# Optimization experiments

Hardware: AMD Instinct MI355X
Metric: run time of the kernel (lower is better)

The kernel has to match this reference:

```python
import jax, jax.numpy as jnp
import numpy as np

TAU = 2.0
HEADS = 8

@jax.custom_vjp
def heaviside(x):
    return (x >= 0).astype(x.dtype)

def _hv_fwd(x):
    return (x >= 0).astype(x.dtype), x

def _hv_bwd(x, g):
    # spikingjelly default surrogate: sigmoid, alpha=4
    s = jax.nn.sigmoid(4.0 * x)
    return (g * 4.0 * s * (1.0 - s),)

heaviside.defvjp(_hv_fwd, _hv_bwd)

def lif(x, v_th=1.0):
    # MultiStepLIFNode(tau=2, v_reset=0, detach_reset, hard reset); x: [T, ...]
    def step(v, xt):
        v = v + (xt - v) / TAU
        s = heaviside(v - v_th)
        v = v * (1.0 - jax.lax.stop_gradient(s))
        return v, s
    _, spikes = jax.lax.scan(step, jnp.zeros_like(x[0]), x)
    return spikes

def bn_c(x, p, eps=1e-5):
    # eval-mode BatchNorm over channel axis 2; p rows: gamma, beta, mean, var
    sh = [1] * x.ndim
    sh[2] = p.shape[1]
    g, b, m, v = (p[i].reshape(sh) for i in range(4))
    return g * (x - m) * jax.lax.rsqrt(v + eps) + b

def setup_inputs():
    key = jax.random.key(0)
    ks = jax.random.split(key, 17)
    T, B, C, H, W = 4, 16, 256, 32, 32
    Hd = 4 * C
    f = lambda k, sh, sc: jax.random.normal(k, sh, jnp.float32) * sc
    u = lambda k, sh: jax.random.uniform(k, sh, jnp.float32)
    return {
        "x": f(ks[0], (T, B, C, H, W), 1.0),
        "res_attn": jnp.zeros((1,), jnp.float32),
        "wq": f(ks[1], (C, C), C ** -0.5),
        "bn_q": u(ks[2], (4, C)),
        "wk": f(ks[3], (C, C), C ** -0.5),
        "bn_k": u(ks[4], (4, C)),
        "wv": f(ks[5], (C, C), C ** -0.5),
        "bn_v": u(ks[6], (4, C)),
        "w_proj": f(ks[7], (C, C), C ** -0.5),
        "b_proj": f(ks[8], (C,), 0.02),
        "bn_proj": u(ks[9], (4, C)),
        "w_fc1": f(ks[10], (Hd, C), C ** -0.5),
        "b_fc1": f(ks[11], (Hd,), 0.02),
        "bn_fc1": u(ks[12], (4, Hd)),
        "w_fc2": f(ks[13], (C, Hd), Hd ** -0.5),
        "b_fc2": f(ks[14], (C,), 0.02),
        "bn_fc2": u(ks[15], (4, C)),
    }

def reference(x, res_attn, wq, bn_q, wk, bn_k, wv, bn_v, w_proj, b_proj, bn_proj,
              w_fc1, b_fc1, bn_fc1, w_fc2, b_fc2, bn_fc2):
    T, B, C, H, W = x.shape
    N = H * W
    d = C // HEADS
    scale = 0.125
    xf = x.reshape(T, B, C, N)

    def qkv(w, bnp):
        y = jnp.einsum('oc,tbcn->tbon', w, xf)  # conv1x1, no bias
        return lif(bn_c(y, bnp))

    # [T,B,C,N] -> [T,B,h,N,d]; channel c = h*d + di (matches torch reshape)
    to_heads = lambda t: t.reshape(T, B, HEADS, d, N).transpose(0, 1, 2, 4, 3)
    q = to_heads(qkv(wq, bn_q))
    k = to_heads(qkv(wk, bn_k))
    v = to_heads(qkv(wv, bn_v))

    kv = jnp.einsum('tbhnd,tbhne->tbhde', k, v)          # [T,B,h,d,d]
    a = jnp.einsum('tbhnd,tbhde->tbhne', q, kv) * scale  # [T,B,h,N,d]
    a = a.transpose(0, 1, 2, 4, 3).reshape(T, B, C, N)   # transpose(3,4)+reshape
    a = lif(a, v_th=0.5)                                 # attn_lif

    p = jnp.einsum('oc,tbcn->tbon', w_proj, a) + b_proj[None, None, :, None]
    attn_out = lif(bn_c(p, bn_proj).reshape(T, B, C, H, W))

    x = x + attn_out

    h1 = jnp.einsum('oc,tbchw->tbohw', w_fc1, x) + b_fc1[None, None, :, None, None]
    h1 = lif(bn_c(h1, bn_fc1))
    h2 = jnp.einsum('co,tbohw->tbchw', w_fc2, h1) + b_fc2[None, None, :, None, None]
    mlp_out = lif(bn_c(h2, bn_fc2))

    return x + mlp_out
```

## Files before the change

kernel.cpp:

```cpp
#include <hip/hip_runtime.h>
#include <stdint.h>

#define T_ 4
#define B_ 16
#define C_ 256
#define N_ 1024
#define HD_ 1024
#define HEADS_ 8
#define DH_ 32

typedef float v2f __attribute__((ext_vector_type(2)));

#define PKL(a, w, x) asm("v_pk_fma_f32 %0, %1, %2, %0 op_sel:[0,0,0] op_sel_hi:[0,1,1]" : "+v"(a) : "v"(w), "v"(x))
#define PKH(a, w, x) asm("v_pk_fma_f32 %0, %1, %2, %0 op_sel:[1,0,0] op_sel_hi:[1,1,1]" : "+v"(a) : "v"(w), "v"(x))

__global__ __launch_bounds__(256)
void transW(const float* __restrict__ W, float* __restrict__ Wt,
            int O, int K, int ostride, int ooff)
{
  __shared__ float tl[32][33];
  int k0 = blockIdx.x*32, o0 = blockIdx.y*32;
  int tid = threadIdx.x;
  int a = tid & 31, bq = tid >> 5;
#pragma unroll
  for (int i=0;i<4;i++)
    tl[bq+8*i][a] = W[(size_t)(o0+bq+8*i)*K + k0 + a];
  __syncthreads();
#pragma unroll
  for (int i=0;i<4;i++)
    Wt[(size_t)(k0+bq+8*i)*ostride + ooff + o0 + a] = tl[a][bq+8*i];
}

__global__ __launch_bounds__(256)
void packBn3(const float* __restrict__ a, const float* __restrict__ b,
             const float* __restrict__ c, float* __restrict__ o)
{
  int i = blockIdx.x*256 + threadIdx.x;
  int r = i >> 8, ci = i & 255;
  o[(size_t)r*768 + ci]       = a[i];
  o[(size_t)r*768 + 256 + ci] = b[i];
  o[(size_t)r*768 + 512 + ci] = c[i];
}

template<typename T> struct VecT;
template<> struct VecT<float>  { using t = float4; };
template<> struct VecT<uint8_t>{ using t = uchar4; };
__device__ __forceinline__ float4 cvt4(float4 v){ return v; }
__device__ __forceinline__ float4 cvt4(uchar4 u){
  return make_float4((float)u.x,(float)u.y,(float)u.z,(float)u.w);
}

template<int KDIM,int ODIM,bool HAS_BIAS,int MODE,typename TIn>
__global__ __launch_bounds__(256,2)
void vec_gemm(const TIn* __restrict__ X, const float* __restrict__ Wt,
              const float* __restrict__ bias, const float* __restrict__ bn,
              const float* __restrict__ resid, void* __restrict__ out, float vth)
{
  using XV = typename VecT<TIn>::t;
  constexpr int NC = KDIM/16;
  __shared__ __align__(16) float Xs[16*128];
  __shared__ __align__(16) float Ws[16*128];

  const int tid = threadIdx.x;
  const int tx = tid & 15, ty = tid >> 4;
  const int b = blockIdx.z, o0 = blockIdx.y*128, n0 = blockIdx.x*128;
  const int sk = tid >> 4, sc = (tid & 15)*8;

  v2f vli[8][4];
#pragma unroll
  for (int i=0;i<8;i++)
#pragma unroll
    for (int j=0;j<4;j++) vli[i][j] = (v2f){0.f,0.f};

  float4 wr0 = *(const float4*)&Wt[(size_t)sk*ODIM + o0+sc];
  float4 wr1 = *(const float4*)&Wt[(size_t)sk*ODIM + o0+sc+4];
  XV xr0 = *(const XV*)(X + (size_t)b*KDIM*N_ + (size_t)sk*N_ + n0+sc);
  XV xr1 = *(const XV*)(X + (size_t)b*KDIM*N_ + (size_t)sk*N_ + n0+sc+4);

  for (int t=0;t<T_;t++){
    v2f acc[8][4];
#pragma unroll
    for (int i=0;i<8;i++)
#pragma unroll
      for (int j=0;j<4;j++) acc[i][j] = (v2f){0.f,0.f};

    for (int c=0;c<NC;c++){
      __syncthreads();
      *(float4*)&Ws[sk*128+sc]   = wr0;
      *(float4*)&Ws[sk*128+sc+4] = wr1;
      *(float4*)&Xs[sk*128+sc]   = cvt4(xr0);
      *(float4*)&Xs[sk*128+sc+4] = cvt4(xr1);
      __syncthreads();
      {
        int nt = t, nc = c+1;
        if (nc==NC){ nc=0; nt=t+1; }
        if (nt<T_){
          const TIn* Xn = X + (size_t)(nt*B_+b)*KDIM*N_;
          wr0 = *(const float4*)&Wt[(size_t)(nc*16+sk)*ODIM + o0+sc];
          wr1 = *(const float4*)&Wt[(size_t)(nc*16+sk)*ODIM + o0+sc+4];
          xr0 = *(const XV*)(Xn + (size_t)(nc*16+sk)*N_ + n0+sc);
          xr1 = *(const XV*)(Xn + (size_t)(nc*16+sk)*N_ + n0+sc+4);
        }
      }
#pragma unroll
      for (int k=0;k<16;k++){
        v2f wa = *(const v2f*)&Ws[k*128 + 8*ty];
        v2f wb = *(const v2f*)&Ws[k*128 + 8*ty + 2];
        v2f wc = *(const v2f*)&Ws[k*128 + 8*ty + 4];
        v2f wd = *(const v2f*)&Ws[k*128 + 8*ty + 6];
        v2f xf[4];
        xf[0] = *(const v2f*)&Xs[k*128 + tx*4];
        xf[1] = *(const v2f*)&Xs[k*128 + tx*4 + 2];
        xf[2] = *(const v2f*)&Xs[k*128 + 64 + tx*4];
        xf[3] = *(const v2f*)&Xs[k*128 + 64 + tx*4 + 2];
#pragma unroll
        for (int j=0;j<4;j++){
          PKL(acc[0][j], wa, xf[j]);
          PKH(acc[1][j], wa, xf[j]);
          PKL(acc[2][j], wb, xf[j]);
          PKH(acc[3][j], wb, xf[j]);
          PKL(acc[4][j], wc, xf[j]);
          PKH(acc[5][j], wc, xf[j]);
          PKL(acc[6][j], wd, xf[j]);
          PKH(acc[7][j], wd, xf[j]);
        }
      }
    }
#pragma unroll
    for (int i=0;i<8;i++){
      int o = o0 + 8*ty + i;
      float g  = bn[o];
      float be = bn[ODIM + o];
      float m  = bn[2*ODIM + o];
      float rs = 1.0f / sqrtf(bn[3*ODIM + o] + 1e-5f);
      float bi = HAS_BIAS ? bias[o] : 0.0f;
      float sv[8];
#pragma unroll
      for (int jj=0;jj<8;jj++){
        float y  = acc[i][jj>>1][jj&1] + bi;
        float yb = (g*(y - m))*rs + be;
        float vv = vli[i][jj>>1][jj&1];
        vv += (yb - vv)*0.5f;
        float s = (vv >= vth) ? 1.0f : 0.0f;
        vli[i][jj>>1][jj&1] = (s!=0.0f) ? 0.0f : vv;
        sv[jj] = s;
      }
      size_t base = ((size_t)(t*B_+b)*ODIM + o)*N_ + n0;
      if (MODE==0){
        uchar4 pa, pb;
        pa.x=(uint8_t)sv[0]; pa.y=(uint8_t)sv[1]; pa.z=(uint8_t)sv[2]; pa.w=(uint8_t)sv[3];
        pb.x=(uint8_t)sv[4]; pb.y=(uint8_t)sv[5]; pb.z=(uint8_t)sv[6]; pb.w=(uint8_t)sv[7];
        *(uchar4*)((uint8_t*)out + base + tx*4)      = pa;
        *(uchar4*)((uint8_t*)out + base + 64 + tx*4) = pb;
      } else {
        float4 r0 = *(const float4*)&resid[base + tx*4];
        float4 r1 = *(const float4*)&resid[base + 64 + tx*4];
        float4 w0 = make_float4(r0.x+sv[0], r0.y+sv[1], r0.z+sv[2], r0.w+sv[3]);
        float4 w1 = make_float4(r1.x+sv[4], r1.y+sv[5], r1.z+sv[6], r1.w+sv[7]);
        *(float4*)&((float*)out)[base + tx*4]      = w0;
        *(float4*)&((float*)out)[base + 64 + tx*4] = w1;
      }
    }
  }
}

__global__ __launch_bounds__(256)
void kv_kernel(const uint8_t* __restrict__ qkv, float* __restrict__ kvout)
{
  int blk = blockIdx.x;
  int h = blk & 7, tb = blk >> 3;
  int tid = threadIdx.x;
  int e = tid & 31, d0 = (tid >> 5) * 4;
  const uint8_t* kp = qkv + ((size_t)tb*768 + 256 + h*DH_)*N_;
  const uint8_t* vp = qkv + ((size_t)tb*768 + 512 + h*DH_)*N_;
  const uint4* vr = (const uint4*)(vp + (size_t)e*N_);
  const uint4* k0 = (const uint4*)(kp + (size_t)(d0+0)*N_);
  const uint4* k1 = (const uint4*)(kp + (size_t)(d0+1)*N_);
  const uint4* k2 = (const uint4*)(kp + (size_t)(d0+2)*N_);
  const uint4* k3 = (const uint4*)(kp + (size_t)(d0+3)*N_);
  int s0=0,s1=0,s2=0,s3=0;
  for (int q=0;q<N_/16;q++){
    uint4 vv = vr[q];
    uint4 a0 = k0[q], a1 = k1[q], a2 = k2[q], a3 = k3[q];
    s0 += __popc(a0.x&vv.x)+__popc(a0.y&vv.y)+__popc(a0.z&vv.z)+__popc(a0.w&vv.w);
    s1 += __popc(a1.x&vv.x)+__popc(a1.y&vv.y)+__popc(a1.z&vv.z)+__popc(a1.w&vv.w);
    s2 += __popc(a2.x&vv.x)+__popc(a2.y&vv.y)+__popc(a2.z&vv.z)+__popc(a2.w&vv.w);
    s3 += __popc(a3.x&vv.x)+__popc(a3.y&vv.y)+__popc(a3.z&vv.z)+__popc(a3.w&vv.w);
  }
  float* kvp = kvout + (size_t)blk*DH_*DH_;
  kvp[(d0+0)*DH_ + e] = (float)s0;
  kvp[(d0+1)*DH_ + e] = (float)s1;
  kvp[(d0+2)*DH_ + e] = (float)s2;
  kvp[(d0+3)*DH_ + e] = (float)s3;
}

__global__ __launch_bounds__(256)
void attn_lif_kernel(const uint8_t* __restrict__ qkv, const float* __restrict__ kv,
                     uint8_t* __restrict__ as_)
{
  int tid = threadIdx.x;
  int n = blockIdx.x*256 + tid;
  int h = blockIdx.y, b = blockIdx.z;
  __shared__ float kvL[DH_*DH_];
  float v[DH_];
#pragma unroll
  for (int e=0;e<DH_;e++) v[e]=0.0f;
  for (int t=0;t<T_;t++){
    const float* kvp = kv + ((size_t)((t*B_+b)*HEADS_+h))*DH_*DH_;
    __syncthreads();
#pragma unroll
    for (int r=0;r<4;r++) kvL[tid+256*r] = kvp[tid+256*r];
    __syncthreads();
    const uint8_t* qp = qkv + ((size_t)(t*B_+b)*768 + h*DH_)*N_ + n;
    float qv[DH_];
#pragma unroll
    for (int d=0;d<DH_;d++) qv[d] = (float)qp[(size_t)d*N_];
    uint8_t* op = as_ + ((size_t)(t*B_+b)*C_ + h*DH_)*N_ + n;
#pragma unroll
    for (int e=0;e<DH_;e++){
      float a=0.0f;
#pragma unroll
      for (int d=0;d<DH_;d++) a += qv[d]*kvL[d*DH_+e];
      a *= 0.125f;
      float vv = v[e];
      vv += (a - vv)*0.5f;
      float s = (vv >= 0.5f) ? 1.0f : 0.0f;
      v[e] = (s!=0.0f) ? 0.0f : vv;
      op[(size_t)e*N_] = (uint8_t)s;
    }
  }
}

extern "C" void kernel_launch(void* const* d_in, const int* in_sizes, int n_in,
                              void* d_out, int out_size, void* d_ws, size_t ws_size,
                              hipStream_t stream)
{
  const float* x      = (const float*)d_in[0];
  const float* wq     = (const float*)d_in[2];
  const float* bn_q   = (const float*)d_in[3];
  const float* wk     = (const float*)d_in[4];
  const float* bn_k   = (const float*)d_in[5];
  const float* wv     = (const float*)d_in[6];
  const float* bn_v   = (const float*)d_in[7];
  const float* wproj  = (const float*)d_in[8];
  const float* bproj  = (const float*)d_in[9];
  const float* bnproj = (const float*)d_in[10];
  const float* wfc1   = (const float*)d_in[11];
  const float* bfc1   = (const float*)d_in[12];
  const float* bnfc1  = (const float*)d_in[13];
  const float* wfc2   = (const float*)d_in[14];
  const float* bfc2   = (const float*)d_in[15];
  const float* bnfc2  = (const float*)d_in[16];

  char* ws = (char*)d_ws;
  const size_t TB = (size_t)T_*B_;
  uint8_t* qkv = (uint8_t*)ws;
  uint8_t* as_ = (uint8_t*)ws + TB*768*N_;
  uint8_t* h1s = (uint8_t*)ws;
  size_t off = TB*768*N_ + TB*(size_t)C_*N_;
  float* xnew = (float*)(ws + off); off += TB*(size_t)C_*N_*4;
  float* WtQ  = (float*)(ws + off); off += (size_t)C_*768*4;
  float* WtP  = (float*)(ws + off); off += (size_t)C_*C_*4;
  float* WtF1 = (float*)(ws + off); off += (size_t)C_*HD_*4;
  float* WtF2 = (float*)(ws + off); off += (size_t)HD_*C_*4;
  float* bnQ  = (float*)(ws + off); off += 4*768*4;
  float* kvb  = (float*)(ws + off); off += TB*HEADS_*DH_*DH_*4;

  dim3 blk(256);
  transW<<<dim3(8,8),blk,0,stream>>>(wq, WtQ, 256, 256, 768, 0);
  transW<<<dim3(8,8),blk,0,stream>>>(wk, WtQ, 256, 256, 768, 256);
  transW<<<dim3(8,8),blk,0,stream>>>(wv, WtQ, 256, 256, 768, 512);
  transW<<<dim3(8,8),blk,0,stream>>>(wproj, WtP, 256, 256, 256, 0);
  transW<<<dim3(8,32),blk,0,stream>>>(wfc1, WtF1, 1024, 256, 1024, 0);
  transW<<<dim3(32,8),blk,0,stream>>>(wfc2, WtF2, 256, 1024, 256, 0);
  packBn3<<<dim3(4),blk,0,stream>>>(bn_q, bn_k, bn_v, bnQ);

  vec_gemm<C_,768,false,0,float><<<dim3(8,6,16),blk,0,stream>>>(
      x, WtQ, nullptr, bnQ, nullptr, qkv, 1.0f);
  kv_kernel<<<dim3(T_*B_*HEADS_),blk,0,stream>>>(qkv, kvb);
  attn_lif_kernel<<<dim3(4,HEADS_,B_),blk,0,stream>>>(qkv, kvb, as_);
  vec_gemm<C_,C_,true,1,uint8_t><<<dim3(8,2,16),blk,0,stream>>>(
      as_, WtP, bproj, bnproj, x, xnew, 1.0f);
  vec_gemm<C_,HD_,true,0,float><<<dim3(8,8,16),blk,0,stream>>>(
      xnew, WtF1, bfc1, bnfc1, nullptr, h1s, 1.0f);
  vec_gemm<HD_,C_,true,1,uint8_t><<<dim3(8,2,16),blk,0,stream>>>(
      h1s, WtF2, bfc2, bnfc2, xnew, d_out, 1.0f);
}
```

Before: 1.539 ms.

## Rewrite pointwise GEMMs to use scalar-register weights and async LDS-staged activations

The register-blocked GEMM with both operands staged in LDS is replaced. In the new kernel each wavefront holds 8 or 16 output-channel weights in scalar registers, loaded with s_load, and applies them to 4 spatial columns per lane with packed FMAs. Activations are double-buffered in LDS through global_load_lds, so the separate register round-trip and LDS store of the weight tile go away. This cuts LDS traffic and VGPR pressure so occupancy can rise to 3 blocks, but each lane now does less work per loaded value and relies on hand-written waitcnt and inline asm being correct.

```diff
diff --git a/kernel.cpp b/kernel.cpp
--- a/kernel.cpp
+++ b/kernel.cpp
@@ -1,5 +1,6 @@
 #include <hip/hip_runtime.h>
 #include <stdint.h>
+#include <math.h>
 
 #define T_ 4
 #define B_ 16
@@ -9,10 +10,13 @@
 #define HEADS_ 8
 #define DH_ 32
 
-typedef float v2f __attribute__((ext_vector_type(2)));
-
-#define PKL(a, w, x) asm("v_pk_fma_f32 %0, %1, %2, %0 op_sel:[0,0,0] op_sel_hi:[0,1,1]" : "+v"(a) : "v"(w), "v"(x))
-#define PKH(a, w, x) asm("v_pk_fma_f32 %0, %1, %2, %0 op_sel:[1,0,0] op_sel_hi:[1,1,1]" : "+v"(a) : "v"(w), "v"(x))
+typedef float v2f  __attribute__((ext_vector_type(2)));
+typedef float f4v  __attribute__((ext_vector_type(4)));
+typedef float f8v  __attribute__((ext_vector_type(8)));
+typedef float f16v __attribute__((ext_vector_type(16)));
+
+#define PKLs(a, w, x) asm volatile("v_pk_fma_f32 %0, %1, %2, %0 op_sel:[0,0,0] op_sel_hi:[0,1,1]" : "+v"(a) : "s"(w), "v"(x))
+#define PKHs(a, w, x) asm volatile("v_pk_fma_f32 %0, %1, %2, %0 op_sel:[1,0,0] op_sel_hi:[1,1,1]" : "+v"(a) : "s"(w), "v"(x))
 
 __global__ __launch_bounds__(256)
 void transW(const float* __restrict__ W, float* __restrict__ Wt,
@@ -42,125 +46,157 @@
   o[(size_t)r*768 + 512 + ci] = c[i];
 }
 
-template<typename T> struct VecT;
-template<> struct VecT<float>  { using t = float4; };
-template<> struct VecT<uint8_t>{ using t = uchar4; };
-__device__ __forceinline__ float4 cvt4(float4 v){ return v; }
-__device__ __forceinline__ float4 cvt4(uchar4 u){
-  return make_float4((float)u.x,(float)u.y,(float)u.z,(float)u.w);
-}
-
-template<int KDIM,int ODIM,bool HAS_BIAS,int MODE,typename TIn>
-__global__ __launch_bounds__(256,2)
-void vec_gemm(const TIn* __restrict__ X, const float* __restrict__ Wt,
-              const float* __restrict__ bias, const float* __restrict__ bn,
-              const float* __restrict__ resid, void* __restrict__ out, float vth)
-{
-  using XV = typename VecT<TIn>::t;
-  constexpr int NC = KDIM/16;
-  __shared__ __align__(16) float Xs[16*128];
-  __shared__ __align__(16) float Ws[16*128];
-
-  const int tid = threadIdx.x;
-  const int tx = tid & 15, ty = tid >> 4;
-  const int b = blockIdx.z, o0 = blockIdx.y*128, n0 = blockIdx.x*128;
-  const int sk = tid >> 4, sc = (tid & 15)*8;
-
-  v2f vli[8][4];
-#pragma unroll
-  for (int i=0;i<8;i++)
-#pragma unroll
-    for (int j=0;j<4;j++) vli[i][j] = (v2f){0.f,0.f};
-
-  float4 wr0 = *(const float4*)&Wt[(size_t)sk*ODIM + o0+sc];
-  float4 wr1 = *(const float4*)&Wt[(size_t)sk*ODIM + o0+sc+4];
-  XV xr0 = *(const XV*)(X + (size_t)b*KDIM*N_ + (size_t)sk*N_ + n0+sc);
-  XV xr1 = *(const XV*)(X + (size_t)b*KDIM*N_ + (size_t)sk*N_ + n0+sc+4);
-
-  for (int t=0;t<T_;t++){
-    v2f acc[8][4];
-#pragma unroll
-    for (int i=0;i<8;i++)
-#pragma unroll
-      for (int j=0;j<4;j++) acc[i][j] = (v2f){0.f,0.f};
-
-    for (int c=0;c<NC;c++){
-      __syncthreads();
-      *(float4*)&Ws[sk*128+sc]   = wr0;
-      *(float4*)&Ws[sk*128+sc+4] = wr1;
-      *(float4*)&Xs[sk*128+sc]   = cvt4(xr0);
-      *(float4*)&Xs[sk*128+sc+4] = cvt4(xr1);
-      __syncthreads();
+template<int UO> struct WReg;
+template<> struct WReg<16> { union { f16v v; v2f p[8]; }; };
+template<> struct WReg<8>  { union { f8v  v; v2f p[4]; }; };
+
+template<int UO>
+__device__ __forceinline__ void wload(WReg<UO>& wr, const float* wp){
+  if constexpr (UO==16)
+    asm volatile("s_load_dwordx16 %0, %1, 0x0" : "=s"(wr.v) : "s"(wp));
+  else
+    asm volatile("s_load_dwordx8 %0, %1, 0x0" : "=s"(wr.v) : "s"(wp));
+}
+
+template<int KDIM,int ODIM,int UO,bool HAS_BIAS,int MODE,typename TIn>
+__global__ __launch_bounds__(256,3)
+void sgemm(const TIn* __restrict__ X, const float* __restrict__ Wt,
+           const float* __restrict__ bias, const float* __restrict__ bn,
+           const float* __restrict__ resid, void* __restrict__ out, float vth)
+{
+  constexpr int NC   = KDIM/16;
+  constexpr int TOT  = T_*NC;
+  constexpr int ESZ  = (int)sizeof(TIn);
+  constexpr int ROWB = 256*ESZ;
+  constexpr int CHB  = 16*ROWB;
+  __shared__ __align__(16) uint8_t LB[2*CHB];
+
+  const int tid  = threadIdx.x;
+  const int lane = tid & 63;
+  const int wid  = __builtin_amdgcn_readfirstlane(tid >> 6);
+  const int b    = blockIdx.z;
+  const int n0   = blockIdx.x*256;
+  const int ow   = blockIdx.y*(4*UO) + wid*UO;
+
+  const uint32_t lbase =
+      (uint32_t)(uintptr_t)(__attribute__((address_space(3))) uint8_t*)&LB[0];
+
+  auto stage = [&](int ch){
+    const int t = ch/NC, c = ch & (NC-1), pb = ch & 1;
+    const TIn* Xb = X + ((size_t)(t*B_+b)*KDIM + c*16)*N_ + n0;
+    if constexpr (ESZ==4){
+#pragma unroll
+      for (int j=0;j<4;j++){
+        const int r = wid + 4*j;
+        __builtin_amdgcn_global_load_lds(
+          (const __attribute__((address_space(1))) void*)(Xb + (size_t)r*N_ + lane*4),
+          (__attribute__((address_space(3))) void*)&LB[pb*CHB + r*ROWB], 16, 0, 0);
+      }
+    } else {
+      const int r = 4*wid + (lane>>4);
+      __builtin_amdgcn_global_load_lds(
+        (const __attribute__((address_space(1))) void*)(Xb + (size_t)r*N_ + (lane&15)*16),
+        (__attribute__((address_space(3))) void*)&LB[pb*CHB + 4*wid*ROWB], 16, 0, 0);
+    }
+  };
+
+  v2f acc[UO][2], vli[UO][2];
+#pragma unroll
+  for (int i=0;i<UO;i++){ vli[i][0]=(v2f){0.f,0.f}; vli[i][1]=(v2f){0.f,0.f}; }
+
+  WReg<UO> w[2];
+  f4v xv[2];
+  uint32_t xw[2];
+
+  stage(0);
+  __syncthreads();
+
+#pragma unroll 1
+  for (int ch=0; ch<TOT; ++ch){
+    const int c  = ch & (NC-1);
+    const int pb = ch & 1;
+    const int kb = c*16;
+
+    if (ch+1 < TOT) stage(ch+1);
+
+    wload<UO>(w[0], Wt + (size_t)kb*ODIM + ow);
+    {
+      uint32_t la = lbase + pb*CHB + lane*(ESZ*4);
+      if constexpr (ESZ==4) asm volatile("ds_read_b128 %0, %1" : "=v"(xv[0]) : "v"(la));
+      else                  asm volatile("ds_read_b32 %0, %1"  : "=v"(xw[0]) : "v"(la));
+    }
+
+    if (c==0){
+#pragma unroll
+      for (int i=0;i<UO;i++){ acc[i][0]=(v2f){0.f,0.f}; acc[i][1]=(v2f){0.f,0.f}; }
+    }
+
+#pragma unroll
+    for (int k=0;k<16;k++){
+      asm volatile("s_waitcnt lgkmcnt(0)" ::: "memory");
+      __builtin_amdgcn_sched_barrier(0);
+      if (k<15){
+        const int s = (k+1)&1;
+        wload<UO>(w[s], Wt + (size_t)(kb+k+1)*ODIM + ow);
+        uint32_t la = lbase + pb*CHB + (k+1)*ROWB + lane*(ESZ*4);
+        if constexpr (ESZ==4) asm volatile("ds_read_b128 %0, %1" : "=v"(xv[s]) : "v"(la));
+        else                  asm volatile("ds_read_b32 %0, %1"  : "=v"(xw[s]) : "v"(la));
+      }
       {
-        int nt = t, nc = c+1;
-        if (nc==NC){ nc=0; nt=t+1; }
-        if (nt<T_){
-          const TIn* Xn = X + (size_t)(nt*B_+b)*KDIM*N_;
-          wr0 = *(const float4*)&Wt[(size_t)(nc*16+sk)*ODIM + o0+sc];
-          wr1 = *(const float4*)&Wt[(size_t)(nc*16+sk)*ODIM + o0+sc+4];
-          xr0 = *(const XV*)(Xn + (size_t)(nc*16+sk)*N_ + n0+sc);
-          xr1 = *(const XV*)(Xn + (size_t)(nc*16+sk)*N_ + n0+sc+4);
+        const int s = k&1;
+        v2f xa, xb;
+        if constexpr (ESZ==4){
+          xa = (v2f){ xv[s][0], xv[s][1] };
+          xb = (v2f){ xv[s][2], xv[s][3] };
+        } else {
+          uint32_t u = xw[s];
+          xa = (v2f){ (float)(u & 255u), (float)((u>>8) & 255u) };
+          xb = (v2f){ (float)((u>>16) & 255u), (float)(u>>24) };
+        }
+#pragma unroll
+        for (int p=0;p<UO/2;p++){
+          PKLs(acc[2*p  ][0], w[s].p[p], xa);
+          PKLs(acc[2*p  ][1], w[s].p[p], xb);
+          PKHs(acc[2*p+1][0], w[s].p[p], xa);
+          PKHs(acc[2*p+1][1], w[s].p[p], xb);
         }
       }
-#pragma unroll
-      for (int k=0;k<16;k++){
-        v2f wa = *(const v2f*)&Ws[k*128 + 8*ty];
-        v2f wb = *(const v2f*)&Ws[k*128 + 8*ty + 2];
-        v2f wc = *(const v2f*)&Ws[k*128 + 8*ty + 4];
-        v2f wd = *(const v2f*)&Ws[k*128 + 8*ty + 6];
-        v2f xf[4];
-        xf[0] = *(const v2f*)&Xs[k*128 + tx*4];
-        xf[1] = *(const v2f*)&Xs[k*128 + tx*4 + 2];
-        xf[2] = *(const v2f*)&Xs[k*128 + 64 + tx*4];
-        xf[3] = *(const v2f*)&Xs[k*128 + 64 + tx*4 + 2];
-#pragma unroll
-        for (int j=0;j<4;j++){
-          PKL(acc[0][j], wa, xf[j]);
-          PKH(acc[1][j], wa, xf[j]);
-          PKL(acc[2][j], wb, xf[j]);
-          PKH(acc[3][j], wb, xf[j]);
-          PKL(acc[4][j], wc, xf[j]);
-          PKH(acc[5][j], wc, xf[j]);
-          PKL(acc[6][j], wd, xf[j]);
-          PKH(acc[7][j], wd, xf[j]);
+    }
+
+    if (c == NC-1){
+      const int t = ch/NC;
+#pragma unroll
+      for (int i=0;i<UO;i++){
+        const int o = ow + i;
+        const float g  = bn[o];
+        const float be = bn[ODIM + o];
+        const float m  = bn[2*ODIM + o];
+        const float rs = 1.0f / sqrtf(bn[3*ODIM + o] + 1e-5f);
+        const float bi = HAS_BIAS ? bias[o] : 0.0f;
+        float sv[4];
+#pragma unroll
+        for (int jj=0;jj<4;jj++){
+          float y  = acc[i][jj>>1][jj&1] + bi;
+          float yb = (g*(y - m))*rs + be;
+          float vv = vli[i][jj>>1][jj&1];
+          vv += (yb - vv)*0.5f;
+          float s = (vv >= vth) ? 1.0f : 0.0f;
+          vli[i][jj>>1][jj&1] = (s!=0.0f) ? 0.0f : vv;
+          sv[jj] = s;
+        }
+        const size_t base = ((size_t)(t*B_+b)*ODIM + o)*N_ + n0 + 4*lane;
+        if (MODE==0){
+          uchar4 pa;
+          pa.x=(uint8_t)sv[0]; pa.y=(uint8_t)sv[1]; pa.z=(uint8_t)sv[2]; pa.w=(uint8_t)sv[3];
+          *(uchar4*)((uint8_t*)out + base) = pa;
+        } else {
+          const float4 r0 = *(const float4*)&resid[base];
+          *(float4*)&((float*)out)[base] =
+            make_float4(r0.x+sv[0], r0.y+sv[1], r0.z+sv[2], r0.w+sv[3]);
         }
       }
     }
-#pragma unroll
-    for (int i=0;i<8;i++){
-      int o = o0 + 8*ty + i;
-      float g  = bn[o];
-      float be = bn[ODIM + o];
-      float m  = bn[2*ODIM + o];
-      float rs = 1.0f / sqrtf(bn[3*ODIM + o] + 1e-5f);
-      float bi = HAS_BIAS ? bias[o] : 0.0f;
-      float sv[8];
-#pragma unroll
-      for (int jj=0;jj<8;jj++){
-        float y  = acc[i][jj>>1][jj&1] + bi;
-        float yb = (g*(y - m))*rs + be;
-        float vv = vli[i][jj>>1][jj&1];
-        vv += (yb - vv)*0.5f;
-        float s = (vv >= vth) ? 1.0f : 0.0f;
-        vli[i][jj>>1][jj&1] = (s!=0.0f) ? 0.0f : vv;
-        sv[jj] = s;
-      }
-      size_t base = ((size_t)(t*B_+b)*ODIM + o)*N_ + n0;
-      if (MODE==0){
-        uchar4 pa, pb;
-        pa.x=(uint8_t)sv[0]; pa.y=(uint8_t)sv[1]; pa.z=(uint8_t)sv[2]; pa.w=(uint8_t)sv[3];
-        pb.x=(uint8_t)sv[4]; pb.y=(uint8_t)sv[5]; pb.z=(uint8_t)sv[6]; pb.w=(uint8_t)sv[7];
-        *(uchar4*)((uint8_t*)out + base + tx*4)      = pa;
-        *(uchar4*)((uint8_t*)out + base + 64 + tx*4) = pb;
-      } else {
-        float4 r0 = *(const float4*)&resid[base + tx*4];
-        float4 r1 = *(const float4*)&resid[base + 64 + tx*4];
-        float4 w0 = make_float4(r0.x+sv[0], r0.y+sv[1], r0.z+sv[2], r0.w+sv[3]);
-        float4 w1 = make_float4(r1.x+sv[4], r1.y+sv[5], r1.z+sv[6], r1.w+sv[7]);
-        *(float4*)&((float*)out)[base + tx*4]      = w0;
-        *(float4*)&((float*)out)[base + 64 + tx*4] = w1;
-      }
-    }
+    __syncthreads();
   }
 }
 
@@ -275,14 +311,14 @@
   transW<<<dim3(32,8),blk,0,stream>>>(wfc2, WtF2, 256, 1024, 256, 0);
   packBn3<<<dim3(4),blk,0,stream>>>(bn_q, bn_k, bn_v, bnQ);
 
-  vec_gemm<C_,768,false,0,float><<<dim3(8,6,16),blk,0,stream>>>(
+  sgemm<C_,768,16,false,0,float><<<dim3(4,12,16),blk,0,stream>>>(
       x, WtQ, nullptr, bnQ, nullptr, qkv, 1.0f);
   kv_kernel<<<dim3(T_*B_*HEADS_),blk,0,stream>>>(qkv, kvb);
   attn_lif_kernel<<<dim3(4,HEADS_,B_),blk,0,stream>>>(qkv, kvb, as_);
-  vec_gemm<C_,C_,true,1,uint8_t><<<dim3(8,2,16),blk,0,stream>>>(
+  sgemm<C_,C_,8,true,1,uint8_t><<<dim3(4,8,16),blk,0,stream>>>(
       as_, WtP, bproj, bnproj, x, xnew, 1.0f);
-  vec_gemm<C_,HD_,true,0,float><<<dim3(8,8,16),blk,0,stream>>>(
+  sgemm<C_,HD_,16,true,0,float><<<dim3(4,16,16),blk,0,stream>>>(
       xnew, WtF1, bfc1, bnfc1, nullptr, h1s, 1.0f);
-  vec_gemm<HD_,C_,true,1,uint8_t><<<dim3(8,2,16),blk,0,stream>>>(
+  sgemm<HD_,C_,8,true,1,uint8_t><<<dim3(4,8,16),blk,0,stream>>>(
       h1s, WtF2, bfc2, bnfc2, xnew, d_out, 1.0f);
 }
```

New measurement: 1.950 ms. 26.8% more time.
